# Optimization experiments

Hardware: AMD Instinct MI355X
Metric: run time of the kernel (lower is better)

The kernel has to match this reference:

```python
import jax, jax.numpy as jnp
import numpy as np

N_JOINTS = 24
IN_PER_J = 4   # in_channels_per_joint
OUT_PER_J = 16 # out_channels_per_joint
IN_CH = N_JOINTS * IN_PER_J    # 96
OUT_CH = N_JOINTS * OUT_PER_J  # 384
BATCH = 262144

# chain skeleton: joint i neighbours {i-1, i, i+1} clipped to range
NEIGHBOUR_LIST = [[j for j in (i - 1, i, i + 1) if 0 <= j < N_JOINTS] for i in range(N_JOINTS)]


def _build_mask():
    mask = np.zeros((OUT_CH, IN_CH), dtype=np.float32)
    for i, neigh in enumerate(NEIGHBOUR_LIST):
        cols = [k * IN_PER_J + d for k in neigh for d in range(IN_PER_J)]
        mask[i * OUT_PER_J:(i + 1) * OUT_PER_J, cols] = 1.0
    return jnp.asarray(mask)


def setup_inputs() -> dict:
    key = jax.random.key(0)
    kx, kw, kb = jax.random.split(key, 3)
    mask = _build_mask()
    fan_in = float(IN_PER_J * 3)  # typical neighbourhood size
    weight = jax.random.normal(kw, (OUT_CH, IN_CH), dtype=jnp.float32) * (1.0 / np.sqrt(fan_in))
    bias = jax.random.uniform(kb, (OUT_CH,), dtype=jnp.float32, minval=-1.0 / np.sqrt(fan_in), maxval=1.0 / np.sqrt(fan_in))
    x = jax.random.normal(kx, (BATCH, IN_CH), dtype=jnp.float32)
    return {"x": x, "weight": weight, "mask": mask, "bias": bias}


def reference(x, weight, mask, bias):
    # flatten trailing dims (input.reshape(B, -1))
    x2 = x.reshape(x.shape[0], -1)              # [B, IN_CH]
    w = weight * mask                           # block-sparse masked weight [OUT_CH, IN_CH]
    return x2 @ w.T + bias                      # F.linear -> [B, OUT_CH]
```

## Files before the change

kernel.cpp:

```cpp
#include <hip/hip_runtime.h>

#define IN_CH 96
#define OUT_CH 384
#define THREADS 384
#define TILE 32

typedef float f32x4 __attribute__((ext_vector_type(4)));
typedef float f32x2 __attribute__((ext_vector_type(2)));

__global__ __launch_bounds__(THREADS, 5) void skel_linear_kernel(
    const float* __restrict__ x,
    const float* __restrict__ weight,
    const float* __restrict__ mask,
    const float* __restrict__ bias,
    float* __restrict__ out,
    int batch)
{
    const int t     = threadIdx.x;
    const int p     = t % 192;
    const int rl    = t / 192;
    const int chan  = p * 2;
    const int joint = p >> 3;
    const int jc    = (joint - 1 < 0) ? 0 : ((joint - 1 > 21) ? 21 : joint - 1);
    const int c0    = jc * 4;

    float w[2][12];
    float b[2];
#pragma unroll
    for (int j = 0; j < 2; ++j) {
        const size_t row = (size_t)(chan + j) * IN_CH;
#pragma unroll
        for (int c = 0; c < 12; ++c)
            w[j][c] = weight[row + c0 + c] * mask[row + c0 + c];
        b[j] = bias[chan + j];
    }
#pragma unroll
    for (int j = 0; j < 2; ++j) {
#pragma unroll
        for (int c = 0; c < 12; ++c)
            asm volatile("" : "+v"(w[j][c]));
        asm volatile("" : "+v"(b[j]));
    }

    __shared__ float xs[TILE * IN_CH];

    const int ntiles = batch / TILE;
    for (int tile = blockIdx.x; tile < ntiles; tile += gridDim.x) {
        const f32x4* src = reinterpret_cast<const f32x4*>(
            x + (size_t)tile * (TILE * IN_CH));
        __syncthreads();
        *reinterpret_cast<f32x4*>(&xs[4 * t])             = src[t];
        *reinterpret_cast<f32x4*>(&xs[4 * (t + THREADS)]) = src[t + THREADS];
        __syncthreads();

        float* outb = out + (size_t)tile * (TILE * OUT_CH) + chan;
#pragma unroll 4
        for (int k = 0; k < TILE / 2; ++k) {
            const int rloc = 2 * k + rl;
            const float* xr = &xs[rloc * IN_CH + c0];
            const f32x4 xa = *reinterpret_cast<const f32x4*>(xr);
            const f32x4 xb = *reinterpret_cast<const f32x4*>(xr + 4);
            const f32x4 xc = *reinterpret_cast<const f32x4*>(xr + 8);

            f32x2 o2;
#pragma unroll
            for (int j = 0; j < 2; ++j) {
                float acc = b[j];
                acc = fmaf(w[j][0],  xa.x, acc);
                acc = fmaf(w[j][1],  xa.y, acc);
                acc = fmaf(w[j][2],  xa.z, acc);
                acc = fmaf(w[j][3],  xa.w, acc);
                acc = fmaf(w[j][4],  xb.x, acc);
                acc = fmaf(w[j][5],  xb.y, acc);
                acc = fmaf(w[j][6],  xb.z, acc);
                acc = fmaf(w[j][7],  xb.w, acc);
                acc = fmaf(w[j][8],  xc.x, acc);
                acc = fmaf(w[j][9],  xc.y, acc);
                acc = fmaf(w[j][10], xc.z, acc);
                acc = fmaf(w[j][11], xc.w, acc);
                o2[j] = acc;
            }

            __builtin_nontemporal_store(o2,
                reinterpret_cast<f32x2*>(outb + (size_t)rloc * OUT_CH));
        }
    }
}

extern "C" void kernel_launch(void* const* d_in, const int* in_sizes, int n_in,
                              void* d_out, int out_size, void* d_ws, size_t ws_size,
                              hipStream_t stream) {
    const float* x      = (const float*)d_in[0];
    const float* weight = (const float*)d_in[1];
    const float* mask   = (const float*)d_in[2];
    const float* bias   = (const float*)d_in[3];
    float* out          = (float*)d_out;

    const int batch = in_sizes[0] / IN_CH;
    const int grid = 1024;

    skel_linear_kernel<<<grid, THREADS, 0, stream>>>(x, weight, mask, bias, out, batch);
}
```

Before: 85.25 us.

## Double-buffer x tiles in LDS with register prefetch of next tile

Loads of the next tile's inputs into registers are issued right after the barrier, so global reads overlap with the FMA and store loop of the current tile. The single LDS tile becomes two, so one barrier per iteration is enough. Each thread now holds more registers and the block uses twice the LDS, which could lower occupancy. On the last iteration the current tile is loaded again as a redundant read.

```diff
diff --git a/kernel.cpp b/kernel.cpp
--- a/kernel.cpp
+++ b/kernel.cpp
@@ -42,48 +42,68 @@
         asm volatile("" : "+v"(b[j]));
     }
 
-    __shared__ float xs[TILE * IN_CH];
+    __shared__ float xs[2][TILE * IN_CH];
 
     const int ntiles = batch / TILE;
-    for (int tile = blockIdx.x; tile < ntiles; tile += gridDim.x) {
+    const int stride = gridDim.x;
+
+    int tile = blockIdx.x;
+    {
         const f32x4* src = reinterpret_cast<const f32x4*>(
             x + (size_t)tile * (TILE * IN_CH));
+    }
+    const f32x4* src0 = reinterpret_cast<const f32x4*>(
+        x + (size_t)tile * (TILE * IN_CH));
+    f32x4 va = src0[t];
+    f32x4 vb = src0[t + THREADS];
+
+    int cur = 0;
+    while (tile < ntiles) {
+        *reinterpret_cast<f32x4*>(&xs[cur][4 * t])             = va;
+        *reinterpret_cast<f32x4*>(&xs[cur][4 * (t + THREADS)]) = vb;
         __syncthreads();
-        *reinterpret_cast<f32x4*>(&xs[4 * t])             = src[t];
-        *reinterpret_cast<f32x4*>(&xs[4 * (t + THREADS)]) = src[t + THREADS];
-        __syncthreads();
+
+        const int tn = tile + stride;
+        const int tc = (tn < ntiles) ? tn : tile;
+        const f32x4* nsrc = reinterpret_cast<const f32x4*>(
+            x + (size_t)tc * (TILE * IN_CH));
+        va = nsrc[t];
+        vb = nsrc[t + THREADS];
 
         float* outb = out + (size_t)tile * (TILE * OUT_CH) + chan;
 #pragma unroll 4
         for (int k = 0; k < TILE / 2; ++k) {
             const int rloc = 2 * k + rl;
-            const float* xr = &xs[rloc * IN_CH + c0];
+            const float* xr = &xs[cur][rloc * IN_CH + c0];
             const f32x4 xa = *reinterpret_cast<const f32x4*>(xr);
-            const f32x4 xb = *reinterpret_cast<const f32x4*>(xr + 4);
+            const f32x4 xb2 = *reinterpret_cast<const f32x4*>(xr + 4);
             const f32x4 xc = *reinterpret_cast<const f32x4*>(xr + 8);
 
             f32x2 o2;
 #pragma unroll
             for (int j = 0; j < 2; ++j) {
                 float acc = b[j];
-                acc = fmaf(w[j][0],  xa.x, acc);
-                acc = fmaf(w[j][1],  xa.y, acc);
-                acc = fmaf(w[j][2],  xa.z, acc);
-                acc = fmaf(w[j][3],  xa.w, acc);
-                acc = fmaf(w[j][4],  xb.x, acc);
-                acc = fmaf(w[j][5],  xb.y, acc);
-                acc = fmaf(w[j][6],  xb.z, acc);
-                acc = fmaf(w[j][7],  xb.w, acc);
-                acc = fmaf(w[j][8],  xc.x, acc);
-                acc = fmaf(w[j][9],  xc.y, acc);
-                acc = fmaf(w[j][10], xc.z, acc);
-                acc = fmaf(w[j][11], xc.w, acc);
+                acc = fmaf(w[j][0],  xa.x,  acc);
+                acc = fmaf(w[j][1],  xa.y,  acc);
+                acc = fmaf(w[j][2],  xa.z,  acc);
+                acc = fmaf(w[j][3],  xa.w,  acc);
+                acc = fmaf(w[j][4],  xb2.x, acc);
+                acc = fmaf(w[j][5],  xb2.y, acc);
+                acc = fmaf(w[j][6],  xb2.z, acc);
+                acc = fmaf(w[j][7],  xb2.w, acc);
+                acc = fmaf(w[j][8],  xc.x,  acc);
+                acc = fmaf(w[j][9],  xc.y,  acc);
+                acc = fmaf(w[j][10], xc.z,  acc);
+                acc = fmaf(w[j][11], xc.w,  acc);
                 o2[j] = acc;
             }
 
             __builtin_nontemporal_store(o2,
                 reinterpret_cast<f32x2*>(outb + (size_t)rloc * OUT_CH));
         }
+
+        cur ^= 1;
+        tile = tn;
     }
 }
 
```

Measured after the change: 87.68 us. +2.9%, slower.
